# Performance work log

Hardware: AMD Instinct MI355X
Metric: run time of the kernel (lower is better)

## Reference

```python
import jax, jax.numpy as jnp
import numpy as np

N_NODES = 50000
N_EDGES = 800000
D_IN = 128
D_OUT = 128


def setup_inputs() -> dict:
    key = jax.random.key(0)
    k1, k2, k3, k4 = jax.random.split(key, 4)
    node_features = jax.random.normal(k1, (N_NODES, D_IN), dtype=jnp.float32)
    edge_index = jax.random.randint(k2, (2, N_EDGES), 0, N_NODES, dtype=jnp.int64)
    # nn.Linear params: weight [out, in], bias [out]
    W = jax.random.normal(k3, (D_OUT, D_IN), dtype=jnp.float32) / np.sqrt(D_IN)
    b = jax.random.normal(k4, (D_OUT,), dtype=jnp.float32) * 0.01
    return {"node_features": node_features, "edge_index": edge_index, "W": W, "b": b}


def reference(node_features, edge_index, W, b):
    source_nodes = edge_index[0]
    dest_nodes = edge_index[1]
    # gather neighbor features [E, D_in], scatter-add into [N, D_in]
    neighbor_features = node_features[source_nodes]
    aggregated = jax.ops.segment_sum(neighbor_features, dest_nodes,
                                     num_segments=node_features.shape[0])
    # nn.Linear: x @ W.T + b
    return aggregated @ W.T + b
```

## Files before the change

### kernel.cpp

```cpp
#include <hip/hip_runtime.h>


constexpr int NN = 50000;
constexpr int NE = 800000;
constexpr int D  = 128;

constexpr int BS   = 128;
constexpr int NB   = (NN + BS - 1) / BS;
constexpr int EPB  = 2048;
constexpr int NSB  = (NE + EPB - 1) / EPB;
constexpr int SUBCAP = 32;
constexpr int CAP  = 4096;

constexpr int AROWU = 136;

typedef __attribute__((ext_vector_type(8))) short bf16x8;
typedef __attribute__((ext_vector_type(4))) float f32x4;

__device__ inline unsigned short f2bf(float f) {
    unsigned u = __float_as_uint(f);
    return (unsigned short)((u + 0x7fffu + ((u >> 16) & 1u)) >> 16);
}
__device__ inline float bflo(unsigned v) { return __uint_as_float(v << 16); }
__device__ inline float bfhi(unsigned v) { return __uint_as_float(v & 0xffff0000u); }

constexpr int NF4 = NN * D / 4;
constexpr int W4  = D * D / 4;
constexpr int NBLK_P = (NF4 + W4 + 255) / 256;
constexpr int GRID_A = NSB + NBLK_P;

__global__ __launch_bounds__(256) void k_prep_bucket(
    const float* __restrict__ nf, const float* __restrict__ W,
    const int* __restrict__ ei,
    ushort* __restrict__ nfh, ushort* __restrict__ Wh,
    ushort* __restrict__ cnt, unsigned* __restrict__ buf)
{
    __shared__ int lcur[NB];
    const int t = threadIdx.x;

    if (blockIdx.x < NSB) {
        const int blk = blockIdx.x;
        for (int i = t; i < NB; i += 256) lcur[i] = 0;
        __syncthreads();
        const int e0 = blk * EPB;
        #pragma unroll
        for (int j = 0; j < 8; ++j) {
            int e = e0 + j * 256 + t;
            if (e < NE) {
                unsigned s = (unsigned)ei[e];
                unsigned d = (unsigned)ei[NE + e];
                unsigned pk = (d << 16) | s;
                int bk = pk >> 23;
                int l = atomicAdd(&lcur[bk], 1);
                if (l < SUBCAP)
                    buf[((size_t)bk * NSB + blk) * SUBCAP + l] = pk;
            }
        }
        __syncthreads();
        for (int i = t; i < NB; i += 256)
            cnt[blk * NB + i] = (ushort)(lcur[i] < SUBCAP ? lcur[i] : SUBCAP);
    } else {
        int i = (blockIdx.x - NSB) * 256 + t;
        if (i < NF4) {
            float4 v = ((const float4*)nf)[i];
            ((ushort4*)nfh)[i] = make_ushort4(f2bf(v.x), f2bf(v.y), f2bf(v.z), f2bf(v.w));
        } else if (i < NF4 + W4) {
            int k = i - NF4;
            float4 v = ((const float4*)W)[k];
            ((ushort4*)Wh)[k] = make_ushort4(f2bf(v.x), f2bf(v.y), f2bf(v.z), f2bf(v.w));
        }
    }
}

__global__ __launch_bounds__(1024) void k_sort_agg(
    const unsigned* __restrict__ nfh, const unsigned* __restrict__ buf,
    const ushort* __restrict__ cnt, const ushort* __restrict__ Wh,
    const float* __restrict__ bias, float* __restrict__ out)
{
    __shared__ unsigned pkbuf[CAP];
    __shared__ ushort srt[CAP];
    __shared__ int scnt[512];
    __shared__ int sbase[NSB];
    __shared__ int hist[BS], off[BS], cur[BS];
    __shared__ unsigned tile[BS * AROWU / 2];
    const int b = blockIdx.x, t = threadIdx.x;
    const int lane = t & 63, w = t >> 6;

    int my = 0;
    if (t < NSB) my = (int)cnt[t * NB + b];
    if (t < 512) scnt[t] = (t < NSB) ? my : 0;
    __syncthreads();
    for (int o = 1; o < 512; o <<= 1) {
        int v = (t >= o && t < 512) ? scnt[t - o] : 0;
        __syncthreads();
        if (t < 512) scnt[t] += v;
        __syncthreads();
    }
    if (t < NSB) sbase[t] = scnt[t] - my;
    if (t < BS) hist[t] = 0;
    __syncthreads();
    int total = scnt[NSB - 1];
    if (total > CAP) total = CAP;

    for (int p = t; p < total; p += 1024) {
        int lo = 0, hi = NSB - 1;
        while (lo < hi) {
            int mid = (lo + hi) >> 1;
            if (scnt[mid] > p) hi = mid; else lo = mid + 1;
        }
        unsigned pk = buf[((size_t)b * NSB + lo) * SUBCAP + (p - sbase[lo])];
        pkbuf[p] = pk;
        atomicAdd(&hist[(pk >> 16) & (BS - 1)], 1);
    }
    __syncthreads();

    if (t < BS) off[t] = hist[t];
    __syncthreads();
    for (int o = 1; o < BS; o <<= 1) {
        int v = (t >= o && t < BS) ? off[t - o] : 0;
        __syncthreads();
        if (t < BS) off[t] += v;
        __syncthreads();
    }
    if (t < BS) { int ex = off[t] - hist[t]; off[t] = ex; cur[t] = ex; }
    __syncthreads();
    for (int e = t; e < total; e += 1024) {
        unsigned pk = pkbuf[e];
        int n = (pk >> 16) & (BS - 1);
        int p = atomicAdd(&cur[n], 1);
        srt[p] = (ushort)(pk & 0xffffu);
    }
    __syncthreads();

    #pragma unroll
    for (int i = 0; i < 8; ++i) {
        const int n = w * 8 + i;
        const int beg = off[n], e = beg + hist[n];
        float ax=0.f, ay=0.f, bx=0.f, by=0.f, cx=0.f, cy=0.f, dx=0.f, dy=0.f;
        for (int p = beg; p < e; p += 8) {
            const int lim = e - 1;
            unsigned v[8];
            #pragma unroll
            for (int j = 0; j < 8; ++j) {
                int pos = p + j;
                bool ok = pos <= lim;
                if (!ok) pos = lim;
                unsigned s = srt[pos];
                unsigned val = nfh[(size_t)s * 64 + lane];
                v[j] = ok ? val : 0u;
            }
            ax += bflo(v[0]); ay += bfhi(v[0]);
            bx += bflo(v[1]); by += bfhi(v[1]);
            cx += bflo(v[2]); cy += bfhi(v[2]);
            dx += bflo(v[3]); dy += bfhi(v[3]);
            ax += bflo(v[4]); ay += bfhi(v[4]);
            bx += bflo(v[5]); by += bfhi(v[5]);
            cx += bflo(v[6]); cy += bfhi(v[6]);
            dx += bflo(v[7]); dy += bfhi(v[7]);
        }
        float rx = (ax + bx) + (cx + dx);
        float ry = (ay + by) + (cy + dy);
        tile[n * (AROWU / 2) + lane] =
            (unsigned)f2bf(rx) | ((unsigned)f2bf(ry) << 16);
    }
    __syncthreads();

    const int m = lane & 15, q = lane >> 4;
    const ushort* lds = (const ushort*)tile;
    #pragma unroll
    for (int i = 0; i < 4; ++i) {
        const int task = w + 16 * i;
        const int t16  = task >> 3;
        const int c0   = (task & 7) * 16;
        const int grow0 = b * BS + t16 * 16;
        if (grow0 < NN) {
            bf16x8 a[4];
            const ushort* arow = lds + (t16 * 16 + m) * AROWU + q * 8;
            #pragma unroll
            for (int kk = 0; kk < 4; ++kk)
                a[kk] = *(const bf16x8*)(arow + kk * 32);
            float bv = bias[c0 + m];
            f32x4 acc = { bv, bv, bv, bv };
            const ushort* wrow = Wh + (size_t)(c0 + m) * D + q * 8;
            #pragma unroll
            for (int kk = 0; kk < 4; ++kk) {
                bf16x8 bb = *(const bf16x8*)(wrow + kk * 32);
                acc = __builtin_amdgcn_mfma_f32_16x16x32_bf16(a[kk], bb, acc, 0, 0, 0);
            }
            float* op = out + (size_t)(grow0 + q * 4) * D + c0 + m;
            op[0]     = acc[0];
            op[D]     = acc[1];
            op[2 * D] = acc[2];
            op[3 * D] = acc[3];
        }
    }
}

extern "C" void kernel_launch(void* const* d_in, const int* in_sizes, int n_in,
                              void* d_out, int out_size, void* d_ws, size_t ws_size,
                              hipStream_t stream) {
    const float* nf = (const float*)d_in[0];
    const int*   ei = (const int*)d_in[1];
    const float* W  = (const float*)d_in[2];
    const float* b  = (const float*)d_in[3];
    float* out = (float*)d_out;

    ushort*   nfh = (ushort*)d_ws;
    ushort*   Wh  = nfh + (size_t)NN * D;
    unsigned* buf = (unsigned*)(Wh + D * D);
    ushort*   cnt = (ushort*)(buf + (size_t)NB * NSB * SUBCAP);

    k_prep_bucket<<<GRID_A, 256, 0, stream>>>(nf, W, ei, nfh, Wh, cnt, buf);
    k_sort_agg   <<<NB, 1024, 0, stream>>>((const unsigned*)nfh, buf, cnt, Wh, b, out);
}
```

Measured before the change: 140.7 us.

## Counting-sort edges per chunk into contiguous buffer with per-bucket offset table

Each edge chunk is now locally counting-sorted by destination bucket in shared memory and written contiguously to a compact buffer. A per-chunk offset table replaces the fixed 32-slot sub-bucket layout. The aggregation kernel reads each bucket's segment from every chunk through those offsets. This removes the large, sparsely filled padded buffer and its scattered global writes, and also removes the silent truncation at 32 edges per sub-bucket. The price is an extra shared-memory histogram, scan and scatter in the prep kernel, with chunk size and block size doubled.

```diff
diff --git a/kernel.cpp b/kernel.cpp
--- a/kernel.cpp
+++ b/kernel.cpp
@@ -7,9 +7,8 @@
 
 constexpr int BS   = 128;
 constexpr int NB   = (NN + BS - 1) / BS;
-constexpr int EPB  = 2048;
+constexpr int EPB  = 4096;
 constexpr int NSB  = (NE + EPB - 1) / EPB;
-constexpr int SUBCAP = 32;
 constexpr int CAP  = 4096;
 
 constexpr int AROWU = 136;
@@ -26,41 +25,68 @@
 
 constexpr int NF4 = NN * D / 4;
 constexpr int W4  = D * D / 4;
-constexpr int NBLK_P = (NF4 + W4 + 255) / 256;
+constexpr int NBLK_P = (NF4 + W4 + 511) / 512;
 constexpr int GRID_A = NSB + NBLK_P;
 
-__global__ __launch_bounds__(256) void k_prep_bucket(
+__global__ __launch_bounds__(512) void k_prep_bucket(
     const float* __restrict__ nf, const float* __restrict__ W,
     const int* __restrict__ ei,
     ushort* __restrict__ nfh, ushort* __restrict__ Wh,
-    ushort* __restrict__ cnt, unsigned* __restrict__ buf)
+    ushort* __restrict__ offs, unsigned* __restrict__ buf)
 {
-    __shared__ int lcur[NB];
+    __shared__ int hist[NB], off[NB], cur[NB];
+    __shared__ unsigned spk[EPB];
     const int t = threadIdx.x;
 
     if (blockIdx.x < NSB) {
         const int blk = blockIdx.x;
-        for (int i = t; i < NB; i += 256) lcur[i] = 0;
-        __syncthreads();
-        const int e0 = blk * EPB;
+        const int e0  = blk * EPB;
+        int cnt = NE - e0; if (cnt > EPB) cnt = EPB;
+
+        for (int i = t; i < NB; i += 512) hist[i] = 0;
+        __syncthreads();
+
+        unsigned pk[8];
         #pragma unroll
         for (int j = 0; j < 8; ++j) {
-            int e = e0 + j * 256 + t;
-            if (e < NE) {
+            int idx = j * 512 + t;
+            if (idx < cnt) {
+                int e = e0 + idx;
                 unsigned s = (unsigned)ei[e];
                 unsigned d = (unsigned)ei[NE + e];
-                unsigned pk = (d << 16) | s;
-                int bk = pk >> 23;
-                int l = atomicAdd(&lcur[bk], 1);
-                if (l < SUBCAP)
-                    buf[((size_t)bk * NSB + blk) * SUBCAP + l] = pk;
-            }
-        }
-        __syncthreads();
-        for (int i = t; i < NB; i += 256)
-            cnt[blk * NB + i] = (ushort)(lcur[i] < SUBCAP ? lcur[i] : SUBCAP);
+                pk[j] = (d << 16) | s;
+                atomicAdd(&hist[pk[j] >> 23], 1);
+            }
+        }
+        __syncthreads();
+        if (t < NB) off[t] = hist[t];
+        __syncthreads();
+        for (int o = 1; o < NB; o <<= 1) {
+            int v = (t >= o && t < NB) ? off[t - o] : 0;
+            __syncthreads();
+            if (t < NB) off[t] += v;
+            __syncthreads();
+        }
+        if (t < NB) {
+            int ex = off[t] - hist[t];
+            cur[t] = ex;
+            offs[blk * (NB + 1) + t] = (ushort)ex;
+        }
+        if (t == 0) offs[blk * (NB + 1) + NB] = (ushort)cnt;
+        __syncthreads();
+        #pragma unroll
+        for (int j = 0; j < 8; ++j) {
+            int idx = j * 512 + t;
+            if (idx < cnt) {
+                int l = atomicAdd(&cur[pk[j] >> 23], 1);
+                spk[l] = pk[j];
+            }
+        }
+        __syncthreads();
+        for (int i = t; i < cnt; i += 512)
+            buf[(size_t)blk * EPB + i] = spk[i];
     } else {
-        int i = (blockIdx.x - NSB) * 256 + t;
+        int i = (blockIdx.x - NSB) * 512 + t;
         if (i < NF4) {
             float4 v = ((const float4*)nf)[i];
             ((ushort4*)nfh)[i] = make_ushort4(f2bf(v.x), f2bf(v.y), f2bf(v.z), f2bf(v.w));
@@ -74,30 +100,35 @@
 
 __global__ __launch_bounds__(1024) void k_sort_agg(
     const unsigned* __restrict__ nfh, const unsigned* __restrict__ buf,
-    const ushort* __restrict__ cnt, const ushort* __restrict__ Wh,
+    const ushort* __restrict__ offs, const ushort* __restrict__ Wh,
     const float* __restrict__ bias, float* __restrict__ out)
 {
     __shared__ unsigned pkbuf[CAP];
     __shared__ ushort srt[CAP];
-    __shared__ int scnt[512];
-    __shared__ int sbase[NSB];
+    __shared__ int scnt[256];
+    __shared__ int sbase[NSB], rbase[NSB];
     __shared__ int hist[BS], off[BS], cur[BS];
     __shared__ unsigned tile[BS * AROWU / 2];
     const int b = blockIdx.x, t = threadIdx.x;
     const int lane = t & 63, w = t >> 6;
 
     int my = 0;
-    if (t < NSB) my = (int)cnt[t * NB + b];
-    if (t < 512) scnt[t] = (t < NSB) ? my : 0;
-    __syncthreads();
-    for (int o = 1; o < 512; o <<= 1) {
-        int v = (t >= o && t < 512) ? scnt[t - o] : 0;
-        __syncthreads();
-        if (t < 512) scnt[t] += v;
+    if (t < NSB) {
+        int o0 = (int)offs[t * (NB + 1) + b];
+        int o1 = (int)offs[t * (NB + 1) + b + 1];
+        rbase[t] = o0;
+        my = o1 - o0;
+    }
+    if (t < 256) scnt[t] = (t < NSB) ? my : 0;
+    if (t < BS) hist[t] = 0;
+    __syncthreads();
+    for (int o = 1; o < 256; o <<= 1) {
+        int v = (t >= o && t < 256) ? scnt[t - o] : 0;
+        __syncthreads();
+        if (t < 256) scnt[t] += v;
         __syncthreads();
     }
     if (t < NSB) sbase[t] = scnt[t] - my;
-    if (t < BS) hist[t] = 0;
     __syncthreads();
     int total = scnt[NSB - 1];
     if (total > CAP) total = CAP;
@@ -108,7 +139,7 @@
             int mid = (lo + hi) >> 1;
             if (scnt[mid] > p) hi = mid; else lo = mid + 1;
         }
-        unsigned pk = buf[((size_t)b * NSB + lo) * SUBCAP + (p - sbase[lo])];
+        unsigned pk = buf[(size_t)lo * EPB + rbase[lo] + (p - sbase[lo])];
         pkbuf[p] = pk;
         atomicAdd(&hist[(pk >> 16) & (BS - 1)], 1);
     }
@@ -205,11 +236,11 @@
     const float* b  = (const float*)d_in[3];
     float* out = (float*)d_out;
 
-    ushort*   nfh = (ushort*)d_ws;
-    ushort*   Wh  = nfh + (size_t)NN * D;
-    unsigned* buf = (unsigned*)(Wh + D * D);
-    ushort*   cnt = (ushort*)(buf + (size_t)NB * NSB * SUBCAP);
-
-    k_prep_bucket<<<GRID_A, 256, 0, stream>>>(nf, W, ei, nfh, Wh, cnt, buf);
-    k_sort_agg   <<<NB, 1024, 0, stream>>>((const unsigned*)nfh, buf, cnt, Wh, b, out);
-}
+    ushort*   nfh  = (ushort*)d_ws;
+    ushort*   Wh   = nfh + (size_t)NN * D;
+    unsigned* buf  = (unsigned*)(Wh + D * D);
+    ushort*   offs = (ushort*)(buf + (size_t)NSB * EPB);
+
+    k_prep_bucket<<<GRID_A, 512, 0, stream>>>(nf, W, ei, nfh, Wh, offs, buf);
+    k_sort_agg   <<<NB, 1024, 0, stream>>>((const unsigned*)nfh, buf, offs, Wh, b, out);
+}
```

New measurement: 136.4 us. -3.1%, faster.
